# Performance work log

Hardware: AMD Instinct MI355X
Metric: run time of the kernel (lower is better)

Reference implementation:

```python
import jax, jax.numpy as jnp
import numpy as np

VOCAB = 100000
DIM = 128
BATCH = 16384
NEG = 10


def setup_inputs() -> dict:
    key = jax.random.key(0)
    k1, k2, k3, k4, k5 = jax.random.split(key, 5)
    init_range = 0.5 / DIM
    focus_W = jax.random.uniform(k1, (VOCAB, DIM), jnp.float32, -init_range, init_range)
    # context_embedding initialized to zeros in the torch code; use tiny random so
    # gradients/outputs are non-degenerate for kernel correctness testing.
    context_W = jax.random.uniform(k2, (VOCAB, DIM), jnp.float32, -init_range, init_range)
    focus_idx = jax.random.randint(k3, (BATCH,), 0, VOCAB, dtype=jnp.int64) if jax.config.read('jax_enable_x64') else jax.random.randint(k3, (BATCH,), 0, VOCAB, dtype=jnp.int32)
    context_idx = jax.random.randint(k4, (BATCH,), 0, VOCAB, dtype=focus_idx.dtype)
    neg_context_idx = jax.random.randint(k5, (BATCH, NEG), 0, VOCAB, dtype=focus_idx.dtype)
    return {
        "focus_W": focus_W,
        "context_W": context_W,
        "focus_idx": focus_idx,
        "context_idx": context_idx,
        "neg_context_idx": neg_context_idx,
    }


def reference(focus_W, context_W, focus_idx, context_idx, neg_context_idx):
    # Embedding gathers: [B, D]
    focus_emb = focus_W[focus_idx]
    ctx_emb = context_W[context_idx]
    # Positive score: per-row dot product -> [B]
    posi_score = jnp.sum(focus_emb * ctx_emb, axis=1)
    posi_predi = jax.nn.log_sigmoid(posi_score)
    # Negative samples: [B, K, D] x [B, D] -> [B, K], then sum over K -> [B]
    neg_ctx_emb = context_W[neg_context_idx]
    neg_score = jnp.einsum("bkd,bd->bk", neg_ctx_emb, focus_emb)
    neg_score = jnp.sum(neg_score, axis=1)
    neg_predi = jax.nn.log_sigmoid(neg_score)
    # Default loss branch: sum((1 - posi_predi)^2) + sum(neg_predi^2)
    loss = jnp.sum(jnp.square(1.0 - posi_predi)) + jnp.sum(jnp.square(neg_predi))
    return loss
```

## Files before the change

kernel.cpp:

```cpp
#include <hip/hip_runtime.h>
#include <math.h>

#define VOCAB 100000
#define DIM   128
#define BATCH 16384
#define NEG   10

__device__ __forceinline__ float logsig(float x) {
    float ax = fabsf(x);
    float l  = log1pf(expf(-ax));
    return (x >= 0.0f) ? -l : (x - l);
}

__global__ __launch_bounds__(256) void sg_partial_kernel(
    const float* __restrict__ focus_W,
    const float* __restrict__ context_W,
    const int*   __restrict__ focus_idx,
    const int*   __restrict__ context_idx,
    const int*   __restrict__ neg_idx,
    float*       __restrict__ partial)
{
    const int t    = threadIdx.x;
    const int sub  = t >> 5;
    const int lane = t & 31;
    const int row  = blockIdx.x * 8 + sub;

    const int fi = focus_idx[row];
    const int ci = context_idx[row];

    const float4 f = *(const float4*)(focus_W   + (size_t)fi * DIM + lane * 4);
    const float4 c = *(const float4*)(context_W + (size_t)ci * DIM + lane * 4);

    float4 ns = make_float4(0.f, 0.f, 0.f, 0.f);
    #pragma unroll
    for (int k = 0; k < NEG; ++k) {
        const int ni = neg_idx[(size_t)row * NEG + k];
        const float4 n = *(const float4*)(context_W + (size_t)ni * DIM + lane * 4);
        ns.x += n.x; ns.y += n.y; ns.z += n.z; ns.w += n.w;
    }

    float pos = f.x * c.x  + f.y * c.y  + f.z * c.z  + f.w * c.w;
    float neg = f.x * ns.x + f.y * ns.y + f.z * ns.z + f.w * ns.w;

    #pragma unroll
    for (int off = 16; off > 0; off >>= 1) {
        pos += __shfl_xor(pos, off);
        neg += __shfl_xor(neg, off);
    }

    __shared__ float s[8];
    if (lane == 0) {
        float pp = logsig(pos);
        float np = logsig(neg);
        s[sub] = (1.0f - pp) * (1.0f - pp) + np * np;
    }
    __syncthreads();
    if (t == 0) {
        float acc = 0.f;
        #pragma unroll
        for (int i = 0; i < 8; ++i) acc += s[i];
        partial[blockIdx.x] = acc;
    }
}

__global__ __launch_bounds__(256) void sg_final_kernel(
    const float* __restrict__ partial, int n, float* __restrict__ out)
{
    float s = 0.0f;
    for (int i = threadIdx.x; i < n; i += 256) s += partial[i];

    #pragma unroll
    for (int off = 32; off > 0; off >>= 1) s += __shfl_xor(s, off);

    __shared__ float ws[4];
    const int wave = threadIdx.x >> 6;
    const int lane = threadIdx.x & 63;
    if (lane == 0) ws[wave] = s;
    __syncthreads();
    if (threadIdx.x == 0) out[0] = (ws[0] + ws[1]) + (ws[2] + ws[3]);
}

extern "C" void kernel_launch(void* const* d_in, const int* in_sizes, int n_in,
                              void* d_out, int out_size, void* d_ws, size_t ws_size,
                              hipStream_t stream) {
    const float* focus_W     = (const float*)d_in[0];
    const float* context_W   = (const float*)d_in[1];
    const int*   focus_idx   = (const int*)d_in[2];
    const int*   context_idx = (const int*)d_in[3];
    const int*   neg_idx     = (const int*)d_in[4];
    float*       out         = (float*)d_out;
    float*       partial     = (float*)d_ws;

    const int blocks = BATCH / 8;

    sg_partial_kernel<<<blocks, 256, 0, stream>>>(
        focus_W, context_W, focus_idx, context_idx, neg_idx, partial);
    sg_final_kernel<<<1, 256, 0, stream>>>(partial, blocks, out);
}
```

Measured before the change: 24.15 us.

## Fuse final reduction into main kernel via last-block atomic ticket

Merges the two-kernel reduction into one kernel: each block writes its partial sum, bumps an atomic counter, and the last block to finish reduces all partials and writes the loss. The negative indices are also loaded up front as int2 pairs into registers. The aim is to remove the second kernel launch and its dependency gap. In exchange it adds a hipMemsetAsync on every call, which is itself a stream operation, plus per-block fences and an atomic.

```diff
diff --git a/kernel.cpp b/kernel.cpp
--- a/kernel.cpp
+++ b/kernel.cpp
@@ -1,10 +1,11 @@
 #include <hip/hip_runtime.h>
 #include <math.h>
 
-#define VOCAB 100000
-#define DIM   128
-#define BATCH 16384
-#define NEG   10
+#define VOCAB  100000
+#define DIM    128
+#define BATCH  16384
+#define NEG    10
+#define NBLOCK (BATCH / 8)
 
 __device__ __forceinline__ float logsig(float x) {
     float ax = fabsf(x);
@@ -12,19 +13,29 @@
     return (x >= 0.0f) ? -l : (x - l);
 }
 
-__global__ __launch_bounds__(256) void sg_partial_kernel(
+__global__ __launch_bounds__(256) void sg_fused_kernel(
     const float* __restrict__ focus_W,
     const float* __restrict__ context_W,
     const int*   __restrict__ focus_idx,
     const int*   __restrict__ context_idx,
     const int*   __restrict__ neg_idx,
-    float*       __restrict__ partial)
+    float*       __restrict__ partial,
+    unsigned*    __restrict__ counter,
+    float*       __restrict__ out)
 {
     const int t    = threadIdx.x;
     const int sub  = t >> 5;
     const int lane = t & 31;
     const int row  = blockIdx.x * 8 + sub;
 
+    const int2* nb = (const int2*)(neg_idx + (size_t)row * NEG);
+    int ni[NEG];
+    #pragma unroll
+    for (int k = 0; k < NEG / 2; ++k) {
+        int2 p = nb[k];
+        ni[2 * k] = p.x;
+        ni[2 * k + 1] = p.y;
+    }
     const int fi = focus_idx[row];
     const int ci = context_idx[row];
 
@@ -34,8 +45,7 @@
     float4 ns = make_float4(0.f, 0.f, 0.f, 0.f);
     #pragma unroll
     for (int k = 0; k < NEG; ++k) {
-        const int ni = neg_idx[(size_t)row * NEG + k];
-        const float4 n = *(const float4*)(context_W + (size_t)ni * DIM + lane * 4);
+        const float4 n = *(const float4*)(context_W + (size_t)ni[k] * DIM + lane * 4);
         ns.x += n.x; ns.y += n.y; ns.z += n.z; ns.w += n.w;
     }
 
@@ -49,35 +59,36 @@
     }
 
     __shared__ float s[8];
+    __shared__ bool  amLast;
     if (lane == 0) {
         float pp = logsig(pos);
         float np = logsig(neg);
         s[sub] = (1.0f - pp) * (1.0f - pp) + np * np;
     }
     __syncthreads();
+
     if (t == 0) {
         float acc = 0.f;
         #pragma unroll
         for (int i = 0; i < 8; ++i) acc += s[i];
         partial[blockIdx.x] = acc;
+        __threadfence();
+        unsigned ticket = atomicAdd(counter, 1u);
+        amLast = (ticket == NBLOCK - 1);
     }
-}
+    __syncthreads();
 
-__global__ __launch_bounds__(256) void sg_final_kernel(
-    const float* __restrict__ partial, int n, float* __restrict__ out)
-{
-    float s = 0.0f;
-    for (int i = threadIdx.x; i < n; i += 256) s += partial[i];
-
-    #pragma unroll
-    for (int off = 32; off > 0; off >>= 1) s += __shfl_xor(s, off);
-
-    __shared__ float ws[4];
-    const int wave = threadIdx.x >> 6;
-    const int lane = threadIdx.x & 63;
-    if (lane == 0) ws[wave] = s;
-    __syncthreads();
-    if (threadIdx.x == 0) out[0] = (ws[0] + ws[1]) + (ws[2] + ws[3]);
+    if (amLast) {
+        __threadfence();
+        float sum = 0.f;
+        for (int i = t; i < NBLOCK; i += 256) sum += partial[i];
+        #pragma unroll
+        for (int off = 32; off > 0; off >>= 1) sum += __shfl_xor(sum, off);
+        __shared__ float ws[4];
+        if ((t & 63) == 0) ws[t >> 6] = sum;
+        __syncthreads();
+        if (t == 0) out[0] = (ws[0] + ws[1]) + (ws[2] + ws[3]);
+    }
 }
 
 extern "C" void kernel_launch(void* const* d_in, const int* in_sizes, int n_in,
@@ -89,11 +100,13 @@
     const int*   context_idx = (const int*)d_in[3];
     const int*   neg_idx     = (const int*)d_in[4];
     float*       out         = (float*)d_out;
-    float*       partial     = (float*)d_ws;
 
-    const int blocks = BATCH / 8;
+    unsigned* counter = (unsigned*)d_ws;
+    float*    partial = (float*)((char*)d_ws + 256);
 
-    sg_partial_kernel<<<blocks, 256, 0, stream>>>(
-        focus_W, context_W, focus_idx, context_idx, neg_idx, partial);
-    sg_final_kernel<<<1, 256, 0, stream>>>(partial, blocks, out);
+    hipMemsetAsync(counter, 0, sizeof(unsigned), stream);
+
+    sg_fused_kernel<<<NBLOCK, 256, 0, stream>>>(
+        focus_W, context_W, focus_idx, context_idx, neg_idx,
+        partial, counter, out);
 }
```

Result: slower. 91.53 us (+279.1%).
